# Performance work log

Measured on AMD Instinct MI355X. Metric: run time of the kernel, lower is better.

Reference implementation:

```python
import jax, jax.numpy as jnp
import numpy as np

B, T, NOBJ = 512, 20, 36
D, V, EMB, E = 2048, 10000, 300, 512
HM, HO = 1024, 256


def setup_inputs() -> dict:
    key = jax.random.key(0)
    ks = jax.random.split(key, 20)
    s = 0.05
    return {
        "obj_enc": jax.random.normal(ks[0], (B, NOBJ, D), jnp.float32),
        "x": jax.random.randint(ks[1], (B, T), 0, V, dtype=jnp.int32),
        "q_means_mask": jax.random.normal(ks[2], (B, T, E), jnp.float32),
        "q_logs_mask": jax.random.normal(ks[3], (B, T, E), jnp.float32) * 0.1,
        "q_z_mask": jax.random.normal(ks[4], (B, T, E), jnp.float32),
        "q_means_obj": jax.random.normal(ks[5], (B, T, E), jnp.float32),
        "q_logs_obj": jax.random.normal(ks[6], (B, T, E), jnp.float32) * 0.1,
        "q_z_obj": jax.random.normal(ks[7], (B, T, E), jnp.float32),
        # learned parameters
        "emd_W": jax.random.normal(ks[8], (V, EMB), jnp.float32) * s,
        "W_ih_m": jax.random.normal(ks[9], (4 * HM, D + E + EMB), jnp.float32) * s,
        "W_hh_m": jax.random.normal(ks[10], (4 * HM, HM), jnp.float32) * s,
        "b_m": jax.random.normal(ks[11], (4 * HM,), jnp.float32) * s,
        "W_ih_o": jax.random.normal(ks[12], (4 * HO, D + 2 * E + EMB), jnp.float32) * s,
        "W_hh_o": jax.random.normal(ks[13], (4 * HO, HO), jnp.float32) * s,
        "b_o": jax.random.normal(ks[14], (4 * HO,), jnp.float32) * s,
        "fc_m_W": jax.random.normal(ks[15], (2 * E, HM), jnp.float32) * s,
        "fc_m_b": jax.random.normal(ks[16], (2 * E,), jnp.float32) * s,
        "fc_o_W": jax.random.normal(ks[17], (2 * E, HO), jnp.float32) * s,
        "fc_o_b": jax.random.normal(ks[18], (2 * E,), jnp.float32) * s,
    }


def _lstm_cell(xt, h, c, W_ih, W_hh, b):
    # torch LSTMCell gate order: i, f, g, o
    g = xt @ W_ih.T + h @ W_hh.T + b
    i, f, gg, o = jnp.split(g, 4, axis=-1)
    c = jax.nn.sigmoid(f) * c + jax.nn.sigmoid(i) * jnp.tanh(gg)
    h = jax.nn.sigmoid(o) * jnp.tanh(c)
    return h, c


def _kl(p_means, p_logs, q_means, q_logs):
    return (0.5 * (p_logs - q_logs)
            + (jnp.exp(q_logs) + (q_means - p_means) ** 2) / (2.0 * jnp.exp(p_logs))
            - 0.5)


def reference(obj_enc, x, q_means_mask, q_logs_mask, q_z_mask,
              q_means_obj, q_logs_obj, q_z_obj,
              emd_W, W_ih_m, W_hh_m, b_m, W_ih_o, W_hh_o, b_o,
              fc_m_W, fc_m_b, fc_o_W, fc_o_b):
    bsz = obj_enc.shape[0]
    # masked mean over object regions
    obj_mask = (jnp.sum(jnp.abs(obj_enc), axis=-1) > 0).astype(obj_enc.dtype)  # [B,N]
    meanimfeats = (obj_enc * obj_mask[..., None]).sum(1) / jnp.maximum(obj_mask.sum(1, keepdims=True), 1e-9)  # [B,D]

    seq_mask = ((x != 0) & (x != 2)).astype(jnp.float32)  # [B,T]
    x_emb = emd_W[x]  # [B,T,EMB]

    # teacher-forced previous latents (zeros at t=0)
    z_m_prev = jnp.concatenate([jnp.zeros_like(q_z_mask[:, :1]), q_z_mask[:, :-1]], axis=1)
    z_o_prev = jnp.concatenate([jnp.zeros_like(q_z_obj[:, :1]), q_z_obj[:, :-1]], axis=1)

    xs = (jnp.swapaxes(x_emb, 0, 1), jnp.swapaxes(z_m_prev, 0, 1),
          jnp.swapaxes(q_z_mask, 0, 1), jnp.swapaxes(z_o_prev, 0, 1))  # time-major

    init = (jnp.zeros((bsz, HM), obj_enc.dtype), jnp.zeros((bsz, HM), obj_enc.dtype),
            jnp.zeros((bsz, HO), obj_enc.dtype), jnp.zeros((bsz, HO), obj_enc.dtype))

    def step(carry, ins):
        h_m, c_m, h_o, c_o = carry
        xt, zmp, zmc, zop = ins
        h_m, c_m = _lstm_cell(jnp.concatenate([zmp, xt, meanimfeats], -1), h_m, c_m, W_ih_m, W_hh_m, b_m)
        out_m = h_m @ fc_m_W.T + fc_m_b  # [B,2E]
        h_o, c_o = _lstm_cell(jnp.concatenate([zmc, zop, xt, meanimfeats], -1), h_o, c_o, W_ih_o, W_hh_o, b_o)
        out_o = h_o @ fc_o_W.T + fc_o_b  # [B,2E]
        return (h_m, c_m, h_o, c_o), (out_m, out_o)

    _, (outs_m, outs_o) = jax.lax.scan(step, init, xs)  # [T,B,2E]
    outs_m = jnp.swapaxes(outs_m, 0, 1)  # [B,T,2E]
    outs_o = jnp.swapaxes(outs_o, 0, 1)

    p_means_mask, p_logs_mask = outs_m[..., :E], outs_m[..., E:]
    p_means_obj, p_logs_obj = outs_o[..., :E], outs_o[..., E:]

    kl_mask = (_kl(p_means_mask, p_logs_mask, q_means_mask, q_logs_mask).sum(-1) * seq_mask).sum(-1)
    kl_obj = (_kl(p_means_obj, p_logs_obj, q_means_obj, q_logs_obj).sum(-1) * seq_mask).sum(-1)
    return kl_mask + kl_obj  # [B]
```

## Files before the change

### kernel.cpp

```cpp
#include <hip/hip_runtime.h>

#define Bz 512
#define Tz 20
#define NOBJz 36
#define Dz 2048
#define EMBz 300
#define Ez 512
#define HMz 1024
#define HOz 256
#define KXM 832
#define KXO 1344

typedef short v8s __attribute__((ext_vector_type(8)));
typedef float v4f __attribute__((ext_vector_type(4)));
typedef unsigned short u16;

__device__ __forceinline__ float sigf(float x) { return 1.f / (1.f + __expf(-x)); }
__device__ __forceinline__ float tanhfast(float x) { return 2.f * sigf(2.f * x) - 1.f; }

__device__ __forceinline__ u16 f2bf(float f) {
    union { float f; unsigned u; } v; v.f = f;
    unsigned u = v.u;
    u += 0x7FFFu + ((u >> 16) & 1u);
    return (u16)(u >> 16);
}
__device__ __forceinline__ float bf2f(u16 h) {
    union { unsigned u; float f; } v; v.u = ((unsigned)h) << 16;
    return v.f;
}


__global__ __launch_bounds__(256) void meanim_fused(const float* __restrict__ obj_enc,
                                                    u16* __restrict__ meanim_bf) {
    const int b = blockIdx.x;
    const int tid = threadIdx.x, lane = tid & 63, w = tid >> 6;
    __shared__ float mask_s[NOBJz];
    for (int n = w; n < NOBJz; n += 4) {
        const float* row = obj_enc + ((size_t)b * NOBJz + n) * Dz;
        float s = 0.f;
        for (int d = lane; d < Dz; d += 64) s += fabsf(row[d]);
        for (int off = 32; off > 0; off >>= 1) s += __shfl_down(s, off);
        if (lane == 0) mask_s[n] = (s > 0.f) ? 1.f : 0.f;
    }
    __syncthreads();
    float cnt = 0.f;
#pragma unroll
    for (int n = 0; n < NOBJz; ++n) cnt += mask_s[n];
    const float inv = 1.f / fmaxf(cnt, 1e-9f);
    for (int d = tid; d < Dz; d += 256) {
        float s = 0.f;
#pragma unroll 4
        for (int n = 0; n < NOBJz; ++n)
            s += obj_enc[((size_t)b * NOBJz + n) * Dz + d] * mask_s[n];
        meanim_bf[(size_t)b * Dz + d] = f2bf(s * inv);
    }
}

__global__ void convert_pad(u16* __restrict__ dst, const float* __restrict__ src,
                            int rows, int src_cols, int ld_src, int col0, int dst_ld, int permH) {
    int idx = blockIdx.x * 256 + threadIdx.x;
    if (idx >= rows * dst_ld) return;
    int rp = idx / dst_ld, c = idx - rp * dst_ld;
    int n = rp;
    if (permH) { int g = (rp >> 4) & 3, u = (rp >> 6) * 16 + (rp & 15); n = g * permH + u; }
    dst[idx] = (c < src_cols) ? f2bf(src[(size_t)n * ld_src + col0 + c]) : (u16)0;
}

__global__ void bias_perm(float* __restrict__ dst, const float* __restrict__ src, int H) {
    int r = blockIdx.x * 256 + threadIdx.x;
    if (r >= 4 * H) return;
    int g = (r >> 4) & 3, u = (r >> 6) * 16 + (r & 15);
    dst[r] = src[g * H + u];
}

__global__ void assemble_Xm(u16* __restrict__ X, const float* __restrict__ qzm,
                            const int* __restrict__ x, const float* __restrict__ emd) {
    int idx = blockIdx.x * 256 + threadIdx.x;
    if (idx >= Tz * Bz * KXM) return;
    int r = idx / KXM, c = idx - r * KXM;
    int t = r / Bz, b = r - t * Bz;
    float v;
    if (c < Ez)             v = (t > 0) ? qzm[((size_t)b * Tz + (t - 1)) * Ez + c] : 0.f;
    else if (c < Ez + EMBz) { int xv = x[b * Tz + t]; v = emd[(size_t)xv * EMBz + (c - Ez)]; }
    else                    v = 0.f;
    X[idx] = f2bf(v);
}

__global__ void assemble_Xo(u16* __restrict__ X, const float* __restrict__ qzm,
                            const float* __restrict__ qzo, const int* __restrict__ x,
                            const float* __restrict__ emd) {
    int idx = blockIdx.x * 256 + threadIdx.x;
    if (idx >= Tz * Bz * KXO) return;
    int r = idx / KXO, c = idx - r * KXO;
    int t = r / Bz, b = r - t * Bz;
    float v;
    if (c < Ez)                 v = qzm[((size_t)b * Tz + t) * Ez + c];
    else if (c < 2 * Ez)        v = (t > 0) ? qzo[((size_t)b * Tz + (t - 1)) * Ez + (c - Ez)] : 0.f;
    else if (c < 2 * Ez + EMBz) { int xv = x[b * Tz + t]; v = emd[(size_t)xv * EMBz + (c - 2 * Ez)]; }
    else                        v = 0.f;
    X[idx] = f2bf(v);
}


#define TILE_E (128 * 64)

__device__ __forceinline__ void stage128(const u16* __restrict__ gA, int lda,
                                         const u16* __restrict__ gW, int ldw,
                                         u16* __restrict__ As, u16* __restrict__ Ws,
                                         int w, int lrow, int lcol) {
#pragma unroll
    for (int c = 0; c < 4; ++c) {
        int chunk = w * 4 + c;
        int row = chunk * 8 + lrow;
        __builtin_amdgcn_global_load_lds(
            (const __attribute__((address_space(1))) unsigned int*)(gA + (size_t)row * lda + lcol),
            (__attribute__((address_space(3))) unsigned int*)(As + chunk * 512), 16, 0, 0);
        __builtin_amdgcn_global_load_lds(
            (const __attribute__((address_space(1))) unsigned int*)(gW + (size_t)row * ldw + lcol),
            (__attribute__((address_space(3))) unsigned int*)(Ws + chunk * 512), 16, 0, 0);
    }
}

__device__ __forceinline__ void mma128(
    const u16* __restrict__ A, int lda, const u16* __restrict__ W, int ldw, int K,
    int bm, int bn, u16* As, u16* Ws, v4f (&acc)[4][4]) {
    const int tid = threadIdx.x;
    const int lane = tid & 63, w = tid >> 6;
    const int wm = w >> 1, wn = w & 1;
    const int r15 = lane & 15, quad = lane >> 4;
    const int lrow = lane >> 3;
    const int lcol = ((lane & 7) ^ lrow) * 8;
    const u16* gA = A + (size_t)bm * lda;
    const u16* gW = W + (size_t)bn * ldw;
    stage128(gA, lda, gW, ldw, As, Ws, w, lrow, lcol);
    __syncthreads();
    int cur = 0;
    for (int k0 = 0; k0 < K; k0 += 64) {
        if (k0 + 64 < K)
            stage128(gA + k0 + 64, lda, gW + k0 + 64, ldw,
                     As + (cur ^ 1) * TILE_E, Ws + (cur ^ 1) * TILE_E, w, lrow, lcol);
        const u16* Asc = As + cur * TILE_E;
        const u16* Wsc = Ws + cur * TILE_E;
#pragma unroll
        for (int kk = 0; kk < 64; kk += 32) {
            v8s a[4], b[4];
#pragma unroll
            for (int i = 0; i < 4; ++i) {
                int r = wm * 64 + 16 * i + r15;
                a[i] = *(const v8s*)&Asc[r * 64 + (((kk >> 3) + quad) ^ (r15 & 7)) * 8];
            }
#pragma unroll
            for (int j = 0; j < 4; ++j) {
                int r = wn * 64 + 16 * j + r15;
                b[j] = *(const v8s*)&Wsc[r * 64 + (((kk >> 3) + quad) ^ (r15 & 7)) * 8];
            }
#pragma unroll
            for (int i = 0; i < 4; ++i)
#pragma unroll
                for (int j = 0; j < 4; ++j)
                    acc[i][j] = __builtin_amdgcn_mfma_f32_16x16x32_bf16(a[i], b[j], acc[i][j], 0, 0, 0);
        }
        __syncthreads();
        cur ^= 1;
    }
}

__global__ __launch_bounds__(256) void gemm128(
    const u16* __restrict__ A, int lda, const u16* __restrict__ W, int ldw,
    void* __restrict__ Cv, int ldc, int K,
    const float* __restrict__ bias, const u16* __restrict__ addR, unsigned addR_mask, int out_bf16) {
    __shared__ u16 As[2 * TILE_E];
    __shared__ u16 Ws[2 * TILE_E];
    v4f acc[4][4] = {};
    const int bm = blockIdx.y * 128, bn = blockIdx.x * 128;
    mma128(A, lda, W, ldw, K, bm, bn, As, Ws, acc);
    const int tid = threadIdx.x, lane = tid & 63, w = tid >> 6;
    const int wm = w >> 1, wn = w & 1, r15 = lane & 15, quad = lane >> 4;
    float* Cf = (float*)Cv;
    u16* Cb = (u16*)Cv;
#pragma unroll
    for (int i = 0; i < 4; ++i)
#pragma unroll
        for (int j = 0; j < 4; ++j) {
            int col = bn + wn * 64 + 16 * j + r15;
            float bv = bias ? bias[col] : 0.f;
#pragma unroll
            for (int r = 0; r < 4; ++r) {
                int row = bm + wm * 64 + 16 * i + quad * 4 + r;
                float v = acc[i][j][r] + bv;
                if (addR) v += bf2f(addR[(size_t)(row & addR_mask) * ldc + col]);
                if (out_bf16) Cb[(size_t)row * ldc + col] = f2bf(v);
                else          Cf[(size_t)row * ldc + col] = v;
            }
        }
}

__global__ __launch_bounds__(256) void step_fused(
    const u16* __restrict__ Hm_prev, const u16* __restrict__ Whh_m, const u16* __restrict__ Gm,
    float* __restrict__ cm, u16* __restrict__ hm,
    const u16* __restrict__ Ho_prev, const u16* __restrict__ Whh_o, const u16* __restrict__ Go,
    float* __restrict__ co, u16* __restrict__ ho) {
    __shared__ u16 As[2 * TILE_E];
    __shared__ u16 Ws[2 * TILE_E];
    v4f acc[4][4] = {};
    const int bx = blockIdx.x;
    const u16 *A, *W, *G;
    float* c;
    u16* h;
    int lda, N4, H, bm, bn, K;
    if (bx < 128) {
        bm = (bx >> 5) * 128; bn = (bx & 31) * 128;
        A = Hm_prev; W = Whh_m; G = Gm; c = cm; h = hm; lda = HMz; N4 = 4 * HMz; H = HMz; K = HMz;
    } else {
        int lx = bx - 128;
        bm = (lx >> 3) * 128; bn = (lx & 7) * 128;
        A = Ho_prev; W = Whh_o; G = Go; c = co; h = ho; lda = HOz; N4 = 4 * HOz; H = HOz; K = HOz;
    }
    mma128(A, lda, W, lda, K, bm, bn, As, Ws, acc);
    const int tid = threadIdx.x, lane = tid & 63, w = tid >> 6;
    const int wm = w >> 1, wn = w & 1, r15 = lane & 15, quad = lane >> 4;
    const int u = ((bn + wn * 64) >> 6) * 16 + r15;
#pragma unroll
    for (int i = 0; i < 4; ++i)
#pragma unroll
        for (int r = 0; r < 4; ++r) {
            int b = bm + wm * 64 + 16 * i + quad * 4 + r;
            size_t gb = (size_t)b * N4 + bn + wn * 64 + r15;
            float gi = acc[i][0][r] + bf2f(G[gb]);
            float gf = acc[i][1][r] + bf2f(G[gb + 16]);
            float gg = acc[i][2][r] + bf2f(G[gb + 32]);
            float go = acc[i][3][r] + bf2f(G[gb + 48]);
            size_t ci = (size_t)b * H + u;
            float cn = sigf(gf) * c[ci] + sigf(gi) * tanhfast(gg);
            c[ci] = cn;
            h[ci] = f2bf(sigf(go) * tanhfast(cn));
        }
}

__global__ void cell0(const u16* __restrict__ Gm, float* __restrict__ cm, u16* __restrict__ hm,
                      const u16* __restrict__ Go, float* __restrict__ co, u16* __restrict__ ho) {
    int idx = blockIdx.x * 256 + threadIdx.x;
    if (idx < Bz * HMz) {
        int b = idx / HMz, u = idx - b * HMz;
        size_t gb = (size_t)b * 4 * HMz + ((u >> 4) * 64 + (u & 15));
        float gi = bf2f(Gm[gb]), gf = bf2f(Gm[gb + 16]), gg = bf2f(Gm[gb + 32]), go = bf2f(Gm[gb + 48]);
        (void)gf;
        float cn = sigf(gi) * tanhfast(gg);
        cm[idx] = cn;
        hm[idx] = f2bf(sigf(go) * tanhfast(cn));
    } else {
        idx -= Bz * HMz;
        if (idx >= Bz * HOz) return;
        int b = idx / HOz, u = idx - b * HOz;
        size_t gb = (size_t)b * 4 * HOz + ((u >> 4) * 64 + (u & 15));
        float gi = bf2f(Go[gb]), gg = bf2f(Go[gb + 32]), go = bf2f(Go[gb + 48]);
        float cn = sigf(gi) * tanhfast(gg);
        co[idx] = cn;
        ho[idx] = f2bf(sigf(go) * tanhfast(cn));
    }
}

__global__ __launch_bounds__(256) void kl_kernel(
    const float* __restrict__ outs_m, const float* __restrict__ outs_o,
    const float* __restrict__ qmm, const float* __restrict__ qlm,
    const float* __restrict__ qmo, const float* __restrict__ qlo,
    const int* __restrict__ x, float* __restrict__ out) {
    int b = blockIdx.x, tid = threadIdx.x;
    float total = 0.f;
    for (int t = 0; t < Tz; ++t) {
        int xv = x[b * Tz + t];
        if (xv == 0 || xv == 2) continue;
        const float* pm = outs_m + ((size_t)t * Bz + b) * 1024;
        const float* po = outs_o + ((size_t)t * Bz + b) * 1024;
        const size_t q = ((size_t)b * Tz + t) * Ez;
        for (int e = tid; e < Ez; e += 256) {
            float pmm = pm[e], plm = pm[Ez + e];
            float dm = qmm[q + e] - pmm;
            total += 0.5f * (plm - qlm[q + e]) + (__expf(qlm[q + e]) + dm * dm) / (2.f * __expf(plm)) - 0.5f;
            float pmo = po[e], plo = po[Ez + e];
            float dn = qmo[q + e] - pmo;
            total += 0.5f * (plo - qlo[q + e]) + (__expf(qlo[q + e]) + dn * dn) / (2.f * __expf(plo)) - 0.5f;
        }
    }
    __shared__ float red[256];
    red[tid] = total;
    __syncthreads();
    for (int s = 128; s > 0; s >>= 1) {
        if (tid < s) red[tid] += red[tid + s];
        __syncthreads();
    }
    if (tid == 0) out[b] = red[0];
}

extern "C" void kernel_launch(void* const* d_in, const int* in_sizes, int n_in,
                              void* d_out, int out_size, void* d_ws, size_t ws_size,
                              hipStream_t stream) {
    const float* obj_enc = (const float*)d_in[0];
    const int*   x       = (const int*)d_in[1];
    const float* qmm     = (const float*)d_in[2];
    const float* qlm     = (const float*)d_in[3];
    const float* qzm     = (const float*)d_in[4];
    const float* qmo     = (const float*)d_in[5];
    const float* qlo     = (const float*)d_in[6];
    const float* qzo     = (const float*)d_in[7];
    const float* emd     = (const float*)d_in[8];
    const float* W_ih_m  = (const float*)d_in[9];
    const float* W_hh_m  = (const float*)d_in[10];
    const float* b_m     = (const float*)d_in[11];
    const float* W_ih_o  = (const float*)d_in[12];
    const float* W_hh_o  = (const float*)d_in[13];
    const float* b_o     = (const float*)d_in[14];
    const float* fc_m_W  = (const float*)d_in[15];
    const float* fc_m_b  = (const float*)d_in[16];
    const float* fc_o_W  = (const float*)d_in[17];
    const float* fc_o_b  = (const float*)d_in[18];
    float* out = (float*)d_out;

    char* base = (char*)d_ws;
    size_t off = 0;
    auto alloc = [&](size_t bytes) { char* r = base + off; off += (bytes + 255) & ~(size_t)255; return r; };
    u16* meanim_bf  = (u16*)alloc((size_t)Bz * Dz * 2);
    u16* Whh_m_bf   = (u16*)alloc((size_t)4 * HMz * HMz * 2);
    u16* Whh_o_bf   = (u16*)alloc((size_t)4 * HOz * HOz * 2);
    u16* Winp_m_bf  = (u16*)alloc((size_t)4 * HMz * KXM * 2);
    u16* Winp_o_bf  = (u16*)alloc((size_t)4 * HOz * KXO * 2);
    u16* Wmean_m_bf = (u16*)alloc((size_t)4 * HMz * Dz * 2);
    u16* Wmean_o_bf = (u16*)alloc((size_t)4 * HOz * Dz * 2);
    u16* Wfc_m_bf   = (u16*)alloc((size_t)1024 * HMz * 2);
    u16* Wfc_o_bf   = (u16*)alloc((size_t)1024 * HOz * 2);
    float* b_m_p    = (float*)alloc((size_t)4 * HMz * 4);
    float* b_o_p    = (float*)alloc((size_t)4 * HOz * 4);
    u16* Xin_m      = (u16*)alloc((size_t)Tz * Bz * KXM * 2);
    u16* Xin_o      = (u16*)alloc((size_t)Tz * Bz * KXO * 2);
    u16* const_m_bf = (u16*)alloc((size_t)Bz * 4 * HMz * 2);
    u16* const_o_bf = (u16*)alloc((size_t)Bz * 4 * HOz * 2);
    u16* Ginp_m_bf  = (u16*)alloc((size_t)Tz * Bz * 4 * HMz * 2);
    u16* Ginp_o_bf  = (u16*)alloc((size_t)Tz * Bz * 4 * HOz * 2);
    float* c_m      = (float*)alloc((size_t)Bz * HMz * 4);
    float* c_o      = (float*)alloc((size_t)Bz * HOz * 4);
    u16* H_m        = (u16*)alloc((size_t)Tz * Bz * HMz * 2);
    u16* H_o        = (u16*)alloc((size_t)Tz * Bz * HOz * 2);
    float* outs_m = (float*)Ginp_m_bf;
    float* outs_o = outs_m + (size_t)Tz * Bz * 1024;

    const int TB = Tz * Bz;

    meanim_fused<<<Bz, 256, 0, stream>>>(obj_enc, meanim_bf);
    assemble_Xm<<<(TB * KXM + 255) / 256, 256, 0, stream>>>(Xin_m, qzm, x, emd);
    assemble_Xo<<<(TB * KXO + 255) / 256, 256, 0, stream>>>(Xin_o, qzm, qzo, x, emd);

    convert_pad<<<(4 * HMz * HMz + 255) / 256, 256, 0, stream>>>(Whh_m_bf, W_hh_m, 4 * HMz, HMz, HMz, 0, HMz, HMz);
    convert_pad<<<(4 * HOz * HOz + 255) / 256, 256, 0, stream>>>(Whh_o_bf, W_hh_o, 4 * HOz, HOz, HOz, 0, HOz, HOz);
    convert_pad<<<(4 * HMz * KXM + 255) / 256, 256, 0, stream>>>(Winp_m_bf, W_ih_m, 4 * HMz, Ez + EMBz, 2860, 0, KXM, HMz);
    convert_pad<<<(4 * HOz * KXO + 255) / 256, 256, 0, stream>>>(Winp_o_bf, W_ih_o, 4 * HOz, 2 * Ez + EMBz, 3372, 0, KXO, HOz);
    convert_pad<<<(4 * HMz * Dz + 255) / 256, 256, 0, stream>>>(Wmean_m_bf, W_ih_m, 4 * HMz, Dz, 2860, Ez + EMBz, Dz, HMz);
    convert_pad<<<(4 * HOz * Dz + 255) / 256, 256, 0, stream>>>(Wmean_o_bf, W_ih_o, 4 * HOz, Dz, 3372, 2 * Ez + EMBz, Dz, HOz);
    convert_pad<<<(1024 * HMz + 255) / 256, 256, 0, stream>>>(Wfc_m_bf, fc_m_W, 1024, HMz, HMz, 0, HMz, 0);
    convert_pad<<<(1024 * HOz + 255) / 256, 256, 0, stream>>>(Wfc_o_bf, fc_o_W, 1024, HOz, HOz, 0, HOz, 0);
    bias_perm<<<(4 * HMz + 255) / 256, 256, 0, stream>>>(b_m_p, b_m, HMz);
    bias_perm<<<(4 * HOz + 255) / 256, 256, 0, stream>>>(b_o_p, b_o, HOz);

    gemm128<<<dim3(4 * HMz / 128, Bz / 128), 256, 0, stream>>>(
        meanim_bf, Dz, Wmean_m_bf, Dz, const_m_bf, 4 * HMz, Dz, b_m_p, nullptr, 0u, 1);
    gemm128<<<dim3(4 * HOz / 128, Bz / 128), 256, 0, stream>>>(
        meanim_bf, Dz, Wmean_o_bf, Dz, const_o_bf, 4 * HOz, Dz, b_o_p, nullptr, 0u, 1);

    gemm128<<<dim3(4 * HMz / 128, TB / 128), 256, 0, stream>>>(
        Xin_m, KXM, Winp_m_bf, KXM, Ginp_m_bf, 4 * HMz, KXM, nullptr, const_m_bf, (unsigned)(Bz - 1), 1);
    gemm128<<<dim3(4 * HOz / 128, TB / 128), 256, 0, stream>>>(
        Xin_o, KXO, Winp_o_bf, KXO, Ginp_o_bf, 4 * HOz, KXO, nullptr, const_o_bf, (unsigned)(Bz - 1), 1);

    cell0<<<(Bz * (HMz + HOz) + 255) / 256, 256, 0, stream>>>(
        Ginp_m_bf, c_m, H_m, Ginp_o_bf, c_o, H_o);

    for (int t = 1; t < Tz; ++t) {
        step_fused<<<160, 256, 0, stream>>>(
            H_m + (size_t)(t - 1) * Bz * HMz, Whh_m_bf, Ginp_m_bf + (size_t)t * Bz * 4 * HMz,
            c_m, H_m + (size_t)t * Bz * HMz,
            H_o + (size_t)(t - 1) * Bz * HOz, Whh_o_bf, Ginp_o_bf + (size_t)t * Bz * 4 * HOz,
            c_o, H_o + (size_t)t * Bz * HOz);
    }

    gemm128<<<dim3(1024 / 128, TB / 128), 256, 0, stream>>>(
        H_m, HMz, Wfc_m_bf, HMz, outs_m, 1024, HMz, fc_m_b, nullptr, 0u, 0);
    gemm128<<<dim3(1024 / 128, TB / 128), 256, 0, stream>>>(
        H_o, HOz, Wfc_o_bf, HOz, outs_o, 1024, HOz, fc_o_b, nullptr, 0u, 0);

    kl_kernel<<<Bz, 256, 0, stream>>>(outs_m, outs_o, qmm, qlm, qmo, qlo, x, out);
}
```

Baseline: 1.424 ms.

## Shrink recurrent step tiles to 64x64 and split mean-image pooling kernels

The per-timestep recurrent GEMM plus LSTM cell kernel moves from 128x128 tiles (160 blocks) to 64x64 tiles (640 blocks). This gives more parallelism across the GPU's compute units on the latency-bound serial loop, at the cost of more redundant loads of the hidden state and weights. Separately, the mean-image computation is split into a per-object mask kernel and a vectorized pooling kernel with many more threads. That adds an extra launch and a small mask buffer.

After: 1.159 ms. -18.6%, faster.

```diff
diff --git a/kernel.cpp b/kernel.cpp
--- a/kernel.cpp
+++ b/kernel.cpp
@@ -30,30 +30,37 @@
 }
 
 
-__global__ __launch_bounds__(256) void meanim_fused(const float* __restrict__ obj_enc,
-                                                    u16* __restrict__ meanim_bf) {
-    const int b = blockIdx.x;
-    const int tid = threadIdx.x, lane = tid & 63, w = tid >> 6;
-    __shared__ float mask_s[NOBJz];
-    for (int n = w; n < NOBJz; n += 4) {
-        const float* row = obj_enc + ((size_t)b * NOBJz + n) * Dz;
-        float s = 0.f;
-        for (int d = lane; d < Dz; d += 64) s += fabsf(row[d]);
-        for (int off = 32; off > 0; off >>= 1) s += __shfl_down(s, off);
-        if (lane == 0) mask_s[n] = (s > 0.f) ? 1.f : 0.f;
-    }
-    __syncthreads();
+__global__ void obj_mask_kernel(const float* __restrict__ obj_enc, float* __restrict__ mask) {
+    int bn = blockIdx.x, lane = threadIdx.x;
+    const v4f* row = (const v4f*)(obj_enc + (size_t)bn * Dz);
+    float s = 0.f;
+    for (int d = lane; d < Dz / 4; d += 64) {
+        v4f v = row[d];
+        s += fabsf(v[0]) + fabsf(v[1]) + fabsf(v[2]) + fabsf(v[3]);
+    }
+    for (int off = 32; off > 0; off >>= 1) s += __shfl_down(s, off);
+    if (lane == 0) mask[bn] = (s > 0.f) ? 1.f : 0.f;
+}
+
+__global__ __launch_bounds__(256) void meanim_kernel(const float* __restrict__ obj_enc,
+                                                     const float* __restrict__ mask,
+                                                     u16* __restrict__ meanim_bf) {
+    int idx = blockIdx.x * 256 + threadIdx.x;
+    if (idx >= Bz * (Dz / 4)) return;
+    int b = idx / (Dz / 4), d4 = idx - b * (Dz / 4);
+    const float* mrow = mask + b * NOBJz;
+    v4f s = {0.f, 0.f, 0.f, 0.f};
     float cnt = 0.f;
-#pragma unroll
-    for (int n = 0; n < NOBJz; ++n) cnt += mask_s[n];
-    const float inv = 1.f / fmaxf(cnt, 1e-9f);
-    for (int d = tid; d < Dz; d += 256) {
-        float s = 0.f;
 #pragma unroll 4
-        for (int n = 0; n < NOBJz; ++n)
-            s += obj_enc[((size_t)b * NOBJz + n) * Dz + d] * mask_s[n];
-        meanim_bf[(size_t)b * Dz + d] = f2bf(s * inv);
-    }
+    for (int n = 0; n < NOBJz; ++n) {
+        float m = mrow[n];
+        cnt += m;
+        v4f v = *(const v4f*)(obj_enc + ((size_t)b * NOBJz + n) * Dz + d4 * 4);
+        s[0] += v[0] * m; s[1] += v[1] * m; s[2] += v[2] * m; s[3] += v[3] * m;
+    }
+    float inv = 1.f / fmaxf(cnt, 1e-9f);
+    u16 o[4] = {f2bf(s[0] * inv), f2bf(s[1] * inv), f2bf(s[2] * inv), f2bf(s[3] * inv)};
+    *(uint2*)&meanim_bf[(size_t)b * Dz + d4 * 4] = *(const uint2*)o;
 }
 
 __global__ void convert_pad(u16* __restrict__ dst, const float* __restrict__ src,
@@ -195,46 +202,102 @@
         }
 }
 
-__global__ __launch_bounds__(256) void step_fused(
+
+#define TILE64_E (64 * 64)
+
+__device__ __forceinline__ void stage64(const u16* __restrict__ gA, int lda,
+                                        const u16* __restrict__ gW, int ldw,
+                                        u16* __restrict__ As, u16* __restrict__ Ws,
+                                        int w, int lrow, int lcol) {
+#pragma unroll
+    for (int c = 0; c < 2; ++c) {
+        int chunk = w * 2 + c;
+        int row = chunk * 8 + lrow;
+        __builtin_amdgcn_global_load_lds(
+            (const __attribute__((address_space(1))) unsigned int*)(gA + (size_t)row * lda + lcol),
+            (__attribute__((address_space(3))) unsigned int*)(As + chunk * 512), 16, 0, 0);
+        __builtin_amdgcn_global_load_lds(
+            (const __attribute__((address_space(1))) unsigned int*)(gW + (size_t)row * ldw + lcol),
+            (__attribute__((address_space(3))) unsigned int*)(Ws + chunk * 512), 16, 0, 0);
+    }
+}
+
+__device__ __forceinline__ void mma64(
+    const u16* __restrict__ A, int lda, const u16* __restrict__ W, int ldw, int K,
+    int bm, int bn, u16* As, u16* Ws, v4f (&acc)[4]) {
+    const int tid = threadIdx.x;
+    const int lane = tid & 63, w = tid >> 6;
+    const int r15 = lane & 15, quad = lane >> 4;
+    const int lrow = lane >> 3;
+    const int lcol = ((lane & 7) ^ lrow) * 8;
+    const u16* gA = A + (size_t)bm * lda;
+    const u16* gW = W + (size_t)bn * ldw;
+    stage64(gA, lda, gW, ldw, As, Ws, w, lrow, lcol);
+    __syncthreads();
+    int cur = 0;
+    for (int k0 = 0; k0 < K; k0 += 64) {
+        if (k0 + 64 < K)
+            stage64(gA + k0 + 64, lda, gW + k0 + 64, ldw,
+                    As + (cur ^ 1) * TILE64_E, Ws + (cur ^ 1) * TILE64_E, w, lrow, lcol);
+        const u16* Asc = As + cur * TILE64_E;
+        const u16* Wsc = Ws + cur * TILE64_E;
+#pragma unroll
+        for (int kk = 0; kk < 64; kk += 32) {
+            const int slot = ((kk >> 3) + quad) ^ (r15 & 7);
+            v8s a, b[4];
+            { int r = w * 16 + r15; a = *(const v8s*)&Asc[r * 64 + slot * 8]; }
+#pragma unroll
+            for (int j = 0; j < 4; ++j) {
+                int r = 16 * j + r15;
+                b[j] = *(const v8s*)&Wsc[r * 64 + slot * 8];
+            }
+#pragma unroll
+            for (int j = 0; j < 4; ++j)
+                acc[j] = __builtin_amdgcn_mfma_f32_16x16x32_bf16(a, b[j], acc[j], 0, 0, 0);
+        }
+        __syncthreads();
+        cur ^= 1;
+    }
+}
+
+__global__ __launch_bounds__(256) void step_fused64(
     const u16* __restrict__ Hm_prev, const u16* __restrict__ Whh_m, const u16* __restrict__ Gm,
     float* __restrict__ cm, u16* __restrict__ hm,
     const u16* __restrict__ Ho_prev, const u16* __restrict__ Whh_o, const u16* __restrict__ Go,
     float* __restrict__ co, u16* __restrict__ ho) {
-    __shared__ u16 As[2 * TILE_E];
-    __shared__ u16 Ws[2 * TILE_E];
-    v4f acc[4][4] = {};
+    __shared__ u16 As[2 * TILE64_E];
+    __shared__ u16 Ws[2 * TILE64_E];
+    v4f acc[4] = {};
     const int bx = blockIdx.x;
     const u16 *A, *W, *G;
     float* c;
     u16* h;
     int lda, N4, H, bm, bn, K;
-    if (bx < 128) {
-        bm = (bx >> 5) * 128; bn = (bx & 31) * 128;
+    if (bx < 512) {
+        bm = (bx >> 6) * 64; bn = (bx & 63) * 64;
         A = Hm_prev; W = Whh_m; G = Gm; c = cm; h = hm; lda = HMz; N4 = 4 * HMz; H = HMz; K = HMz;
     } else {
-        int lx = bx - 128;
-        bm = (lx >> 3) * 128; bn = (lx & 7) * 128;
+        int lx = bx - 512;
+        bm = (lx >> 4) * 64; bn = (lx & 15) * 64;
         A = Ho_prev; W = Whh_o; G = Go; c = co; h = ho; lda = HOz; N4 = 4 * HOz; H = HOz; K = HOz;
     }
-    mma128(A, lda, W, lda, K, bm, bn, As, Ws, acc);
+    mma64(A, lda, W, lda, K, bm, bn, As, Ws, acc);
     const int tid = threadIdx.x, lane = tid & 63, w = tid >> 6;
-    const int wm = w >> 1, wn = w & 1, r15 = lane & 15, quad = lane >> 4;
-    const int u = ((bn + wn * 64) >> 6) * 16 + r15;
-#pragma unroll
-    for (int i = 0; i < 4; ++i)
-#pragma unroll
-        for (int r = 0; r < 4; ++r) {
-            int b = bm + wm * 64 + 16 * i + quad * 4 + r;
-            size_t gb = (size_t)b * N4 + bn + wn * 64 + r15;
-            float gi = acc[i][0][r] + bf2f(G[gb]);
-            float gf = acc[i][1][r] + bf2f(G[gb + 16]);
-            float gg = acc[i][2][r] + bf2f(G[gb + 32]);
-            float go = acc[i][3][r] + bf2f(G[gb + 48]);
-            size_t ci = (size_t)b * H + u;
-            float cn = sigf(gf) * c[ci] + sigf(gi) * tanhfast(gg);
-            c[ci] = cn;
-            h[ci] = f2bf(sigf(go) * tanhfast(cn));
-        }
+    const int r15 = lane & 15, quad = lane >> 4;
+    const int u = (bn >> 6) * 16 + r15;
+#pragma unroll
+    for (int r = 0; r < 4; ++r) {
+        int bidx = bm + w * 16 + quad * 4 + r;
+        size_t gb = (size_t)bidx * N4 + bn + r15;
+        float gi = acc[0][r] + bf2f(G[gb]);
+        float gf = acc[1][r] + bf2f(G[gb + 16]);
+        float gg = acc[2][r] + bf2f(G[gb + 32]);
+        float go = acc[3][r] + bf2f(G[gb + 48]);
+        size_t ci = (size_t)bidx * H + u;
+        float cn = sigf(gf) * c[ci] + sigf(gi) * tanhfast(gg);
+        c[ci] = cn;
+        h[ci] = f2bf(sigf(go) * tanhfast(cn));
+    }
 }
 
 __global__ void cell0(const u16* __restrict__ Gm, float* __restrict__ cm, u16* __restrict__ hm,
@@ -243,8 +306,7 @@
     if (idx < Bz * HMz) {
         int b = idx / HMz, u = idx - b * HMz;
         size_t gb = (size_t)b * 4 * HMz + ((u >> 4) * 64 + (u & 15));
-        float gi = bf2f(Gm[gb]), gf = bf2f(Gm[gb + 16]), gg = bf2f(Gm[gb + 32]), go = bf2f(Gm[gb + 48]);
-        (void)gf;
+        float gi = bf2f(Gm[gb]), gg = bf2f(Gm[gb + 32]), go = bf2f(Gm[gb + 48]);
         float cn = sigf(gi) * tanhfast(gg);
         cm[idx] = cn;
         hm[idx] = f2bf(sigf(go) * tanhfast(cn));
@@ -319,6 +381,7 @@
     char* base = (char*)d_ws;
     size_t off = 0;
     auto alloc = [&](size_t bytes) { char* r = base + off; off += (bytes + 255) & ~(size_t)255; return r; };
+    float* mask     = (float*)alloc((size_t)Bz * NOBJz * 4);
     u16* meanim_bf  = (u16*)alloc((size_t)Bz * Dz * 2);
     u16* Whh_m_bf   = (u16*)alloc((size_t)4 * HMz * HMz * 2);
     u16* Whh_o_bf   = (u16*)alloc((size_t)4 * HOz * HOz * 2);
@@ -345,7 +408,8 @@
 
     const int TB = Tz * Bz;
 
-    meanim_fused<<<Bz, 256, 0, stream>>>(obj_enc, meanim_bf);
+    obj_mask_kernel<<<Bz * NOBJz, 64, 0, stream>>>(obj_enc, mask);
+    meanim_kernel<<<(Bz * (Dz / 4) + 255) / 256, 256, 0, stream>>>(obj_enc, mask, meanim_bf);
     assemble_Xm<<<(TB * KXM + 255) / 256, 256, 0, stream>>>(Xin_m, qzm, x, emd);
     assemble_Xo<<<(TB * KXO + 255) / 256, 256, 0, stream>>>(Xin_o, qzm, qzo, x, emd);
 
@@ -374,7 +438,7 @@
         Ginp_m_bf, c_m, H_m, Ginp_o_bf, c_o, H_o);
 
     for (int t = 1; t < Tz; ++t) {
-        step_fused<<<160, 256, 0, stream>>>(
+        step_fused64<<<640, 256, 0, stream>>>(
             H_m + (size_t)(t - 1) * Bz * HMz, Whh_m_bf, Ginp_m_bf + (size_t)t * Bz * 4 * HMz,
             c_m, H_m + (size_t)t * Bz * HMz,
             H_o + (size_t)(t - 1) * Bz * HOz, Whh_o_bf, Ginp_o_bf + (size_t)t * Bz * 4 * HOz,
```
